# Optimization experiments

Hardware: AMD Instinct MI355X
Metric: run time of the kernel (lower is better)

The kernel has to match this reference:

```python
import jax, jax.numpy as jnp
import numpy as np

DN = ('NCHW', 'OIHW', 'NCHW')
B, T, D, H, W = 8, 10, 10, 128, 128
WINDOW_OUT = 5


def conv2d(x, w, b):
    y = jax.lax.conv_general_dilated(x, w, (1, 1), 'SAME', dimension_numbers=DN)
    return y + b[None, :, None, None]


def lstm_cell(x, h, c, w, b):
    # ConvLSTM gate update: conv over [x; h], split into i,f,o,g
    z = conv2d(jnp.concatenate([x, h], axis=1), w, b)
    i, f, o, g = jnp.split(z, 4, axis=1)
    c2 = jax.nn.sigmoid(f) * c + jax.nn.sigmoid(i) * jnp.tanh(g)
    h2 = jax.nn.sigmoid(o) * jnp.tanh(c2)
    return h2, c2


def attn_score(x, h, c, w1, b1, w2, b2):
    # conv-MLP attention score over concat([x, h, c]) -> (b, H, W)
    z = jnp.concatenate([x, h, c], axis=1)
    return conv2d(jnp.tanh(conv2d(z, w1, b1)), w2, b2)[:, 0]


def setup_inputs():
    key = jax.random.key(0)
    ks = jax.random.split(key, 16)
    s = 0.05
    return {
        'x': jax.random.normal(ks[0], (B, T, D, H, W), jnp.float32),
        'h0': jnp.zeros((B, 1, H, W), jnp.float32),
        'c0': jnp.zeros((B, 1, H, W), jnp.float32),
        'h1': jnp.zeros((B, 64, H, W), jnp.float32),
        'c1': jnp.zeros((B, 64, H, W), jnp.float32),
        # encoder cells: layer0 (in 10, hid 1), layer1 (in 1, hid 64)
        'w_enc0': jax.random.normal(ks[1], (4, 11, 3, 3), jnp.float32) * s,
        'b_enc0': jax.random.normal(ks[2], (4,), jnp.float32) * s,
        'w_enc1': jax.random.normal(ks[3], (256, 65, 3, 3), jnp.float32) * s,
        'b_enc1': jax.random.normal(ks[4], (256,), jnp.float32) * s,
        # decoder cells: layer0 (in 1, hid 64), layer1 (in 64, hid 1)
        'w_dec0': jax.random.normal(ks[5], (256, 65, 3, 3), jnp.float32) * s,
        'b_dec0': jax.random.normal(ks[6], (256,), jnp.float32) * s,
        'w_dec1': jax.random.normal(ks[7], (4, 65, 3, 3), jnp.float32) * s,
        'b_dec1': jax.random.normal(ks[8], (4,), jnp.float32) * s,
        # input attention: in 10+2*1=12 -> 32 -> 1
        'wa1': jax.random.normal(ks[9], (32, 12, 3, 3), jnp.float32) * s,
        'ba1': jax.random.normal(ks[10], (32,), jnp.float32) * s,
        'wa2': jax.random.normal(ks[11], (1, 32, 3, 3), jnp.float32) * s,
        'ba2': jax.random.normal(ks[12], (1,), jnp.float32) * s,
        # temporal attention: in 1+2*64=129 -> 32 -> 1
        'wt1': jax.random.normal(ks[13], (32, 129, 3, 3), jnp.float32) * s,
        'bt1': jax.random.normal(ks[14], (32,), jnp.float32) * s,
        'wt2': jax.random.normal(ks[15], (1, 32, 3, 3), jnp.float32) * s,
        'bt2': jnp.zeros((1,), jnp.float32),
    }


def reference(x, h0, c0, h1, c1, w_enc0, b_enc0, w_enc1, b_enc1,
              w_dec0, b_dec0, w_dec1, b_dec1,
              wa1, ba1, wa2, ba2, wt1, bt1, wt2, bt2):
    def input_attn(xx, h, c):
        # per-feature score; vmap over feature dim k (axis 2 of x)
        score = jax.vmap(lambda xk: attn_score(xk, h, c, wa1, ba1, wa2, ba2),
                         in_axes=2, out_axes=1)(xx)          # (b, D, H, W)
        alpha = jax.nn.softmax(score, axis=1)
        return xx * alpha[:, None]                            # broadcast over time

    # ---- encoder layer 0: input attention re-weights x every step (compounding)
    def step0(carry, t):
        xx, h, c = carry
        xx = input_attn(xx, h, c)
        h, c = lstm_cell(xx[:, t], h, c, w_enc0, b_enc0)
        return (xx, h, c), (h, c)

    _, (hs0, cs0) = jax.lax.scan(step0, (x, h0, c0), jnp.arange(T))
    hs0 = jnp.moveaxis(hs0, 0, 1)   # (b, T, 1, H, W)
    cs0 = jnp.moveaxis(cs0, 0, 1)

    # ---- encoder layer 1
    def step1(carry, xt):
        h, c = lstm_cell(xt, carry[0], carry[1], w_enc1, b_enc1)
        return (h, c), (h, c)

    _, (hs1, cs1) = jax.lax.scan(step1, (h1, c1), jnp.moveaxis(hs0, 1, 0))
    hs1 = jnp.moveaxis(hs1, 0, 1)   # (b, T, 64, H, W)
    cs1 = jnp.moveaxis(cs1, 0, 1)

    def temporal_attn(y, hb, cb):
        score = jax.vmap(lambda ht, ct: attn_score(y, ht, ct, wt1, bt1, wt2, bt2),
                         in_axes=1, out_axes=1)(hb, cb)       # (b, T, H, W)
        beta = jax.nn.softmax(score, axis=1)
        return jnp.sum(hb * beta[:, :, None], axis=1), cb[:, -1]

    # ---- decoder: states reversed -> layer0 uses encoder layer1 states, etc.
    y0 = x[:, -1, 0][:, None]       # x[:, [-1], selected_dim] -> (b, 1, H, W)

    def dec_step(carry, _):
        y, hb0, cb0, hb1, cb1 = carry
        ht, ct = temporal_attn(y, hb0, cb0)
        ht, ct = lstm_cell(y, ht, ct, w_dec0, b_dec0)
        y = ht
        hb0 = jnp.concatenate([hb0[:, 1:], ht[:, None]], axis=1)
        cb0 = jnp.concatenate([cb0[:, 1:], ct[:, None]], axis=1)
        ht2, ct2 = lstm_cell(y, hb1[:, -1], cb1[:, -1], w_dec1, b_dec1)
        y = ht2
        hb1 = jnp.concatenate([hb1[:, 1:], ht2[:, None]], axis=1)
        cb1 = jnp.concatenate([cb1[:, 1:], ct2[:, None]], axis=1)
        return (y, hb0, cb0, hb1, cb1), y

    _, ys = jax.lax.scan(dec_step, (y0, hs1, cs1, hs0, cs0), None, length=WINDOW_OUT)
    return jnp.moveaxis(ys, 0, 1)   # (b, window_out, 1, H, W)
```

## Files before the change

kernel.cpp:

```cpp
#include <hip/hip_runtime.h>


#define PX 16384L
#define T_ 10
#define D_ 10

__device__ __forceinline__ float fast_tanh(float x) {
    const float e = __builtin_exp2f(x * 2.88539008f);
    return 1.f - 2.f * __builtin_amdgcn_rcpf(e + 1.f);
}
__device__ __forceinline__ float fast_sig(float x) {
    const float e = __builtin_exp2f(x * -1.44269504f);
    return __builtin_amdgcn_rcpf(e + 1.f);
}
__device__ __forceinline__ float fast_exp(float x) {
    return __builtin_exp2f(x * 1.44269504f);
}

__device__ __forceinline__ void lstm_dev(
    float* lds,
    int tile, int hcb, int b,
    const float* __restrict__ in0, long bs0,
    const float* __restrict__ in1,
    const float* __restrict__ w, const float* __restrict__ bias,
    const float* __restrict__ cprev,
    float* __restrict__ hout, float* __restrict__ cout_)
{
    const int tid = threadIdx.x;
    const int tx = tid & 31, r0 = (tid >> 5) << 1;
    const int tileX = (tile & 3) << 5, tileY = (tile >> 2) << 4;
    const int hc0 = hcb << 1;
    float acc[16];
#pragma unroll
    for (int j = 0; j < 16; j++) acc[j] = 0.f;

    int g0[3]; float m0[3];
#pragma unroll
    for (int i = 0; i < 3; i++) {
        const int lidx = tid + i * 256;
        const int r = lidx / 34, cc = lidx - r * 34;
        const int gy = tileY + r - 1, gx = tileX + cc - 1;
        const bool inb = (lidx < 612) && ((unsigned)gy < 128u) && ((unsigned)gx < 128u);
        g0[i] = inb ? gy * 128 + gx : 0;
        m0[i] = inb ? 1.f : 0.f;
    }

    for (int cb = 0; cb < 65; cb += 8) {
        const int cmax = min(8, 65 - cb);
        for (int cl = 0; cl < cmax; cl++) {
            const int ci = cb + cl;
            const float* p = (ci == 0) ? in0 + (long)b * bs0
                                       : in1 + ((long)b * 64 + (ci - 1)) * PX;
#pragma unroll
            for (int i = 0; i < 3; i++) {
                const int lidx = tid + i * 256;
                if (lidx < 612) lds[cl * 612 + lidx] = m0[i] * p[g0[i]];
            }
        }
        __syncthreads();
        for (int cl = 0; cl < cmax; cl++) {
            float win[4][3];
#pragma unroll
            for (int dy = 0; dy < 4; dy++)
#pragma unroll
                for (int dx = 0; dx < 3; dx++)
                    win[dy][dx] = lds[cl * 612 + (r0 + dy) * 34 + tx + dx];
            const int ci = cb + cl;
#pragma unroll
            for (int j = 0; j < 2; j++)
#pragma unroll
                for (int g = 0; g < 4; g++) {
                    const float* wp = w + ((long)(g * 64 + hc0 + j) * 65 + ci) * 9;
#pragma unroll
                    for (int rr = 0; rr < 2; rr++) {
                        float a = acc[(j * 4 + g) * 2 + rr];
#pragma unroll
                        for (int ky = 0; ky < 3; ky++)
#pragma unroll
                            for (int kx = 0; kx < 3; kx++)
                                a = fmaf(wp[ky * 3 + kx], win[rr + ky][kx], a);
                        acc[(j * 4 + g) * 2 + rr] = a;
                    }
                }
        }
        __syncthreads();
    }
#pragma unroll
    for (int j = 0; j < 2; j++) {
        const int hc = hc0 + j;
        const float bi = bias[hc], bf = bias[64 + hc];
        const float bo = bias[128 + hc], bg = bias[192 + hc];
#pragma unroll
        for (int rr = 0; rr < 2; rr++) {
            const long opix = (long)(tileY + r0 + rr) * 128 + tileX + tx;
            const float i_ = fast_sig(acc[(j * 4 + 0) * 2 + rr] + bi);
            const float f_ = fast_sig(acc[(j * 4 + 1) * 2 + rr] + bf);
            const float o_ = fast_sig(acc[(j * 4 + 2) * 2 + rr] + bo);
            const float g_ = fast_tanh(acc[(j * 4 + 3) * 2 + rr] + bg);
            const float cp = cprev[((long)b * 64 + hc) * PX + opix];
            const float c2 = f_ * cp + i_ * g_;
            const float h2 = o_ * fast_tanh(c2);
            hout[((long)b * 64 + hc) * PX + opix] = h2;
            cout_[((long)b * 64 + hc) * PX + opix] = c2;
        }
    }
}

__device__ __forceinline__ void zpart_dev(
    float* lds,
    int tile, int cob, int b,
    const float* __restrict__ hsrc, const float* __restrict__ csrc,
    const float* __restrict__ wt1, const float* __restrict__ bt1,
    float* __restrict__ zdst)
{
    const int tid = threadIdx.x;
    const int tx = tid & 15, ty = tid >> 4;
    const int tileX = (tile & 7) << 4, tileY = (tile >> 3) << 4;
    const int co0 = cob << 3;
    float acc[8];
#pragma unroll
    for (int j = 0; j < 8; j++) acc[j] = 0.f;

    int g0[2]; float m0[2];
#pragma unroll
    for (int i = 0; i < 2; i++) {
        const int lidx = tid + i * 256;
        const int r = lidx / 18, cc = lidx - r * 18;
        const int gy = tileY + r - 1, gx = tileX + cc - 1;
        const bool inb = (lidx < 324) && ((unsigned)gy < 128u) && ((unsigned)gx < 128u);
        g0[i] = inb ? gy * 128 + gx : 0;
        m0[i] = inb ? 1.f : 0.f;
    }

    for (int cb = 0; cb < 128; cb += 4) {
        for (int cl = 0; cl < 4; cl++) {
            const int ci = cb + cl;
            const float* p = (ci < 64) ? hsrc + ((long)b * 64 + ci) * PX
                                       : csrc + ((long)b * 64 + (ci - 64)) * PX;
#pragma unroll
            for (int i = 0; i < 2; i++) {
                const int lidx = tid + i * 256;
                if (lidx < 324) lds[cl * 324 + lidx] = m0[i] * p[g0[i]];
            }
        }
        __syncthreads();
        for (int cl = 0; cl < 4; cl++) {
            float r9[9];
#pragma unroll
            for (int dy = 0; dy < 3; dy++)
#pragma unroll
                for (int dx = 0; dx < 3; dx++)
                    r9[dy * 3 + dx] = lds[cl * 324 + (ty + dy) * 18 + tx + dx];
            const int ci = cb + cl;
#pragma unroll
            for (int j = 0; j < 8; j++) {
                const float* wp = wt1 + ((long)(co0 + j) * 129 + 1 + ci) * 9;
                float a = acc[j];
#pragma unroll
                for (int q = 0; q < 9; q++) a = fmaf(wp[q], r9[q], a);
                acc[j] = a;
            }
        }
        __syncthreads();
    }
    const long opix = (long)(tileY + ty) * 128 + tileX + tx;
#pragma unroll
    for (int j = 0; j < 8; j++)
        zdst[((long)b * 32 + co0 + j) * PX + opix] = acc[j] + bt1[co0 + j];
}

__global__ __launch_bounds__(256)
void lstm_merge_k(const float* __restrict__ in0, long bs0,
                  const float* __restrict__ in1,
                  const float* __restrict__ w, const float* __restrict__ bias,
                  const float* __restrict__ cprev,
                  float* __restrict__ hout, float* __restrict__ cout_,
                  const float* __restrict__ zh, const float* __restrict__ zc,
                  float* __restrict__ zdst,
                  const float* __restrict__ wt1, const float* __restrict__ bt1)
{
    __shared__ float lds[8 * 612];
    const int bid = blockIdx.x, b = blockIdx.z;
    if (bid < 1024) {
        lstm_dev(lds, bid & 31, bid >> 5, b, in0, bs0, in1, w, bias,
                 cprev, hout, cout_);
    } else {
        const int q = bid - 1024;
        zpart_dev(lds, q & 63, q >> 6, b, zh, zc, wt1, bt1, zdst);
    }
}

__global__ __launch_bounds__(256)
void zpart_k(const float* __restrict__ zh, const float* __restrict__ zc,
             float* __restrict__ zdst,
             const float* __restrict__ wt1, const float* __restrict__ bt1)
{
    __shared__ float lds[4 * 324];
    zpart_dev(lds, blockIdx.x, blockIdx.y, blockIdx.z, zh, zc, wt1, bt1, zdst);
}

__global__ __launch_bounds__(256)
void dec_merge_k(const float* __restrict__ hs1s,
                 const float* __restrict__ hb1, long hb1bs,
                 const float* __restrict__ w1,
                 float* __restrict__ l1p, int nb,
                 const float* __restrict__ zc, float* __restrict__ zdst,
                 const float* __restrict__ wt1, const float* __restrict__ bt1)
{
    __shared__ float lds[4 * 324];
    const int bid = blockIdx.x, b = blockIdx.z;
    if (bid < 256) {
        const int tile = bid & 63, s = bid >> 6;
        const int ci0 = (s == 0) ? 0 : (s == 1) ? 17 : (s == 2) ? 33 : 49;
        const int cn  = (s == 0) ? 17 : 16;
        const int tid = threadIdx.x;
        const int tx = tid & 15, ty = tid >> 4;
        const int tileX = (tile & 7) << 4, tileY = (tile >> 3) << 4;
        int g0[2]; float m0[2];
#pragma unroll
        for (int i = 0; i < 2; i++) {
            const int lidx = tid + i * 256;
            const int r = lidx / 18, cc = lidx - r * 18;
            const int gy = tileY + r - 1, gx = tileX + cc - 1;
            const bool inb = (lidx < 324) && ((unsigned)gy < 128u) && ((unsigned)gx < 128u);
            g0[i] = inb ? gy * 128 + gx : 0;
            m0[i] = inb ? 1.f : 0.f;
        }
        float acc[4] = {0.f, 0.f, 0.f, 0.f};
        for (int cb = 0; cb < cn; cb += 4) {
            const int cmax = min(4, cn - cb);
            for (int cl = 0; cl < cmax; cl++) {
                const int ci = ci0 + cb + cl;
                const float* p = (ci < 64) ? hs1s + ((long)b * 64 + ci) * PX
                                           : hb1 + (long)b * hb1bs;
#pragma unroll
                for (int i = 0; i < 2; i++) {
                    const int lidx = tid + i * 256;
                    if (lidx < 324) lds[cl * 324 + lidx] = m0[i] * p[g0[i]];
                }
            }
            __syncthreads();
            for (int cl = 0; cl < cmax; cl++) {
                float r9[9];
#pragma unroll
                for (int dy = 0; dy < 3; dy++)
#pragma unroll
                    for (int dx = 0; dx < 3; dx++)
                        r9[dy * 3 + dx] = lds[cl * 324 + (ty + dy) * 18 + tx + dx];
                const int ci = ci0 + cb + cl;
#pragma unroll
                for (int j = 0; j < 4; j++) {
                    const float* wp = w1 + ((long)j * 65 + ci) * 9;
                    float a = acc[j];
#pragma unroll
                    for (int q = 0; q < 9; q++) a = fmaf(wp[q], r9[q], a);
                    acc[j] = a;
                }
            }
            __syncthreads();
        }
        const long opix = (long)(tileY + ty) * 128 + tileX + tx;
#pragma unroll
        for (int j = 0; j < 4; j++)
            l1p[(((long)s * nb + b) * 4 + j) * PX + opix] = acc[j];
    } else {
        const int q = bid - 256;
        zpart_dev(lds, q & 63, q >> 6, b, hs1s, zc, wt1, bt1, zdst);
    }
}

__global__ __launch_bounds__(256)
void combine_lstm_k(const float* __restrict__ pbuf, int nsl, int hidden,
                    const float* __restrict__ bias,
                    const float* __restrict__ cprev, long cpbs,
                    float* __restrict__ hout, long hobs,
                    float* __restrict__ cout_, long cobs,
                    float* __restrict__ hout2, long ho2bs, int nb)
{
    const long idx = (long)blockIdx.x * 256 + threadIdx.x;
    if (idx >= (long)nb * hidden * PX) return;
    const long px = idx & 16383;
    const long v = idx >> 14;
    const int hc = (int)(v % hidden), b = (int)(v / hidden);
    const int nco = 4 * hidden;
    float g4[4] = {0.f, 0.f, 0.f, 0.f};
    for (int s = 0; s < nsl; s++)
#pragma unroll
        for (int g = 0; g < 4; g++)
            g4[g] += pbuf[(((long)s * nb + b) * nco + g * hidden + hc) * PX + px];
    const float i_ = fast_sig(g4[0] + bias[hc]);
    const float f_ = fast_sig(g4[1] + bias[hidden + hc]);
    const float o_ = fast_sig(g4[2] + bias[2 * hidden + hc]);
    const float g_ = fast_tanh(g4[3] + bias[3 * hidden + hc]);
    const float cp = cprev[(long)b * cpbs + (long)hc * PX + px];
    const float c2 = f_ * cp + i_ * g_;
    const float h2 = o_ * fast_tanh(c2);
    hout[(long)b * hobs + (long)hc * PX + px] = h2;
    cout_[(long)b * cobs + (long)hc * PX + px] = c2;
    if (hout2) hout2[(long)b * ho2bs + (long)hc * PX + px] = h2;
}

__global__ __launch_bounds__(256)
void enc0_lstm_k(const float* __restrict__ x, int t, const float* __restrict__ A,
                 const float* __restrict__ hprev, const float* __restrict__ cprev,
                 const float* __restrict__ w, const float* __restrict__ bias,
                 float* __restrict__ hout, float* __restrict__ cout_)
{
    __shared__ float lds[4 * 324];
    const int tid = threadIdx.x;
    const int tx = tid & 15, ty = tid >> 4;
    const int tile = blockIdx.x, b = blockIdx.z;
    const int tileX = (tile & 7) << 4, tileY = (tile >> 3) << 4;
    int g0[2]; float m0[2]; float aTr[2][10];
#pragma unroll
    for (int i = 0; i < 2; i++) {
        const int lidx = tid + i * 256;
        const int r = lidx / 18, cc = lidx - r * 18;
        const int gy = tileY + r - 1, gx = tileX + cc - 1;
        const bool inb = (lidx < 324) && ((unsigned)gy < 128u) && ((unsigned)gx < 128u);
        g0[i] = inb ? gy * 128 + gx : 0;
        m0[i] = inb ? 1.f : 0.f;
    }
    float acc[4] = {0.f, 0.f, 0.f, 0.f};
    for (int cb = 0; cb < 11; cb += 4) {
        const int cmax = min(4, 11 - cb);
        for (int cl = 0; cl < cmax; cl++) {
            const int ci = cb + cl;
#pragma unroll
            for (int i = 0; i < 2; i++) {
                const int lidx = tid + i * 256;
                if (lidx < 324) {
                    float v;
                    if (ci < 10) {
                        v = x[(((long)b * T_ + t) * D_ + ci) * PX + g0[i]]
                            * A[((long)b * 10 + ci) * PX + g0[i]];
                    } else {
                        v = hprev[(long)b * PX + g0[i]];
                    }
                    lds[cl * 324 + lidx] = m0[i] * v;
                }
            }
        }
        __syncthreads();
        for (int cl = 0; cl < cmax; cl++) {
            float r9[9];
#pragma unroll
            for (int dy = 0; dy < 3; dy++)
#pragma unroll
                for (int dx = 0; dx < 3; dx++)
                    r9[dy * 3 + dx] = lds[cl * 324 + (ty + dy) * 18 + tx + dx];
            const int ci = cb + cl;
#pragma unroll
            for (int g = 0; g < 4; g++) {
                const float* wp = w + ((long)g * 11 + ci) * 9;
                float a = acc[g];
#pragma unroll
                for (int q = 0; q < 9; q++) a = fmaf(wp[q], r9[q], a);
                acc[g] = a;
            }
        }
        __syncthreads();
    }
    const long opix = (long)(tileY + ty) * 128 + tileX + tx;
    const float i_ = fast_sig(acc[0] + bias[0]);
    const float f_ = fast_sig(acc[1] + bias[1]);
    const float o_ = fast_sig(acc[2] + bias[2]);
    const float g_ = fast_tanh(acc[3] + bias[3]);
    const float cp = cprev[(long)b * PX + opix];
    const float c2 = f_ * cp + i_ * g_;
    const float h2 = o_ * fast_tanh(c2);
    hout[(long)b * PX + opix] = h2;
    cout_[(long)b * PX + opix] = c2;
}

__global__ __launch_bounds__(256)
void iattn_k(const float* __restrict__ x, const float* __restrict__ A,
             const float* __restrict__ h, const float* __restrict__ c,
             const float* __restrict__ wa1, const float* __restrict__ ba1,
             const float* __restrict__ wa2, const float* __restrict__ ba2,
             float* __restrict__ score)
{
    __shared__ float xl[12][400];
    __shared__ float zl[16][324];
    const int tid = threadIdx.x;
    const int tileX = (blockIdx.x & 7) << 4, tileY = (blockIdx.x >> 3) << 4;
    const int z = blockIdx.z;
    const int b = z & 7, k = z >> 3;

    int g0[2]; float m0[2]; float aTr[2];
#pragma unroll
    for (int i = 0; i < 2; i++) {
        const int lidx = tid + i * 256;
        const int r = lidx / 20, cc = lidx - r * 20;
        const int gy = tileY + r - 2, gx = tileX + cc - 2;
        const bool inb = (lidx < 400) && ((unsigned)gy < 128u) && ((unsigned)gx < 128u);
        g0[i] = inb ? gy * 128 + gx : 0;
        m0[i] = inb ? 1.f : 0.f;
        aTr[i] = A ? (m0[i] * A[((long)b * 10 + k) * PX + g0[i]]) : 1.f;
    }
    for (int ch = 0; ch < 12; ch++) {
        const float* p = (ch < 10) ? x + (((long)b * 10 + ch) * 10 + k) * PX
                       : (ch == 10) ? h + (long)b * PX : c + (long)b * PX;
#pragma unroll
        for (int i = 0; i < 2; i++) {
            const int lidx = tid + i * 256;
            if (lidx < 400) {
                float v = m0[i] * p[g0[i]];
                if (ch < 10) v *= aTr[i];
                xl[ch][lidx] = v;
            }
        }
    }
    __syncthreads();

    const int i0 = tid;
    const int i1 = tid + 256;
    const int zr0 = i0 / 18, zc0 = i0 - zr0 * 18;
    const int zr1 = (i1 < 324) ? i1 / 18 : 0;
    const int zc1 = (i1 < 324) ? i1 - zr1 * 18 : 0;
    const int gy0 = tileY + zr0 - 1, gx0 = tileX + zc0 - 1;
    const bool in0_ = (i0 < 324) && ((unsigned)gy0 < 128u) && ((unsigned)gx0 < 128u);
    const int gy1 = tileY + zr1 - 1, gx1 = tileX + zc1 - 1;
    const bool in1_ = (i1 < 324) && ((unsigned)gy1 < 128u) && ((unsigned)gx1 < 128u);

    const int tx = tid & 15, ty = tid >> 4;
    float sacc = ba2[0];

    for (int hf = 0; hf < 2; hf++) {
        float acc0[16], acc1[16];
#pragma unroll
        for (int co = 0; co < 16; co++) { acc0[co] = 0.f; acc1[co] = 0.f; }
        for (int ci = 0; ci < 12; ci++) {
            float wA[9], wB[9];
#pragma unroll
            for (int dy = 0; dy < 3; dy++)
#pragma unroll
                for (int dx = 0; dx < 3; dx++) {
                    wA[dy * 3 + dx] = xl[ci][(zr0 + dy) * 20 + zc0 + dx];
                    wB[dy * 3 + dx] = xl[ci][(zr1 + dy) * 20 + zc1 + dx];
                }
#pragma unroll
            for (int co = 0; co < 16; co++) {
                const float* wp = wa1 + ((long)(hf * 16 + co) * 12 + ci) * 9;
                float a0 = acc0[co], a1 = acc1[co];
#pragma unroll
                for (int q = 0; q < 9; q++) {
                    a0 = fmaf(wp[q], wA[q], a0);
                    a1 = fmaf(wp[q], wB[q], a1);
                }
                acc0[co] = a0; acc1[co] = a1;
            }
        }
        if (hf) __syncthreads();
#pragma unroll
        for (int co = 0; co < 16; co++) {
            zl[co][i0] = in0_ ? fast_tanh(acc0[co] + ba1[hf * 16 + co]) : 0.f;
            if (i1 < 324) zl[co][i1] = in1_ ? fast_tanh(acc1[co] + ba1[hf * 16 + co]) : 0.f;
        }
        __syncthreads();
        for (int co = 0; co < 16; co++) {
            const float* wp = wa2 + (hf * 16 + co) * 9;
#pragma unroll
            for (int ky = 0; ky < 3; ky++)
#pragma unroll
                for (int kx = 0; kx < 3; kx++)
                    sacc = fmaf(wp[ky * 3 + kx], zl[co][(ty + ky) * 18 + tx + kx], sacc);
        }
    }
    score[((long)b * 10 + k) * PX + (long)(tileY + ty) * 128 + tileX + tx] = sacc;
}

__global__ __launch_bounds__(256)
void softmax_mul_k(const float* __restrict__ s, float* __restrict__ A, int nb, int init)
{
    const long idx = (long)blockIdx.x * 256 + threadIdx.x;
    if (idx >= (long)nb * PX) return;
    const long b = idx >> 14, p = idx & 16383;
    const float* base = s + b * 10 * PX + p;
    float v[10]; float m = -1e30f;
#pragma unroll
    for (int t = 0; t < 10; t++) { v[t] = base[t * PX]; m = fmaxf(m, v[t]); }
    float sum = 0.f;
#pragma unroll
    for (int t = 0; t < 10; t++) { v[t] = fast_exp(v[t] - m); sum += v[t]; }
    const float r = __builtin_amdgcn_rcpf(sum);
    float* Ab = A + b * 10 * PX + p;
#pragma unroll
    for (int t = 0; t < 10; t++)
        Ab[t * PX] = init ? (v[t] * r) : (Ab[t * PX] * v[t] * r);
}

__global__ __launch_bounds__(256)
void attn_fuse_k(const float* __restrict__ y, long ybs,
                 const float* __restrict__ zpart,
                 const float* __restrict__ wt1,
                 const float* __restrict__ wt2, const float* __restrict__ bt2,
                 float* __restrict__ score, int nb)
{
    __shared__ float ylds[400];
    __shared__ float zl[16][324];
    const int tid = threadIdx.x;
    const int tileX = (blockIdx.x & 7) << 4, tileY = (blockIdx.x >> 3) << 4;
    const int z = blockIdx.z;
    const int b = z % nb, t = z / nb;

#pragma unroll
    for (int i = 0; i < 2; i++) {
        const int lidx = tid + i * 256;
        if (lidx < 400) {
            const int r = lidx / 20, cc = lidx - r * 20;
            const int gy = tileY + r - 2, gx = tileX + cc - 2;
            const bool inb = ((unsigned)gy < 128u) && ((unsigned)gx < 128u);
            ylds[lidx] = inb ? y[(long)b * ybs + gy * 128 + gx] : 0.f;
        }
    }
    __syncthreads();

    const int i0 = tid, i1 = tid + 256;
    const int zr0 = i0 / 18, zc0 = i0 - zr0 * 18;
    const int zr1 = (i1 < 324) ? i1 / 18 : 0;
    const int zc1 = (i1 < 324) ? i1 - zr1 * 18 : 0;
    const int gy0 = tileY + zr0 - 1, gx0 = tileX + zc0 - 1;
    const bool in0_ = ((unsigned)gy0 < 128u) && ((unsigned)gx0 < 128u);
    const int gy1 = tileY + zr1 - 1, gx1 = tileX + zc1 - 1;
    const bool in1_ = (i1 < 324) && ((unsigned)gy1 < 128u) && ((unsigned)gx1 < 128u);
    const long pix0 = in0_ ? (long)gy0 * 128 + gx0 : 0;
    const long pix1 = in1_ ? (long)gy1 * 128 + gx1 : 0;
    const float* zp0 = zpart + ((long)t * nb + b) * 32 * PX;

    const int tx = tid & 15, ty = tid >> 4;
    float sacc = bt2[0];

    for (int hf = 0; hf < 2; hf++) {
        float yw0[9], yw1[9];
#pragma unroll
        for (int dy = 0; dy < 3; dy++)
#pragma unroll
            for (int dx = 0; dx < 3; dx++) {
                yw0[dy * 3 + dx] = ylds[(zr0 + dy) * 20 + zc0 + dx];
                yw1[dy * 3 + dx] = ylds[(zr1 + dy) * 20 + zc1 + dx];
            }
        if (hf) __syncthreads();
#pragma unroll 4
        for (int ch = 0; ch < 16; ch++) {
            const int cg = hf * 16 + ch;
            const float* wy = wt1 + (long)cg * 129 * 9;
            float s0 = zp0[(long)cg * PX + pix0];
            float s1 = (i1 < 324) ? zp0[(long)cg * PX + pix1] : 0.f;
#pragma unroll
            for (int q = 0; q < 9; q++) {
                s0 = fmaf(wy[q], yw0[q], s0);
                s1 = fmaf(wy[q], yw1[q], s1);
            }
            zl[ch][i0] = in0_ ? fast_tanh(s0) : 0.f;
            if (i1 < 324) zl[ch][i1] = in1_ ? fast_tanh(s1) : 0.f;
        }
        __syncthreads();
        for (int ch = 0; ch < 16; ch++) {
            const float* wp = wt2 + (hf * 16 + ch) * 9;
#pragma unroll
            for (int ky = 0; ky < 3; ky++)
#pragma unroll
                for (int kx = 0; kx < 3; kx++)
                    sacc = fmaf(wp[ky * 3 + kx], zl[ch][(ty + ky) * 18 + tx + kx], sacc);
        }
    }
    score[((long)b * 10 + t) * PX + (long)(tileY + ty) * 128 + tileX + tx] = sacc;
}

__global__ __launch_bounds__(256)
void smax_wsum_k(const float* __restrict__ score, const float* __restrict__ hs1,
                 float* __restrict__ aht, int nb)
{
    const long idx = (long)blockIdx.x * 256 + threadIdx.x;
    if (idx >= (long)nb * PX) return;
    const long b = idx >> 14, p = idx & 16383;
    const int ch0 = blockIdx.y * 8;
    const float* base = score + b * 10 * PX + p;
    float v[10]; float m = -1e30f;
#pragma unroll
    for (int t = 0; t < 10; t++) { v[t] = base[t * PX]; m = fmaxf(m, v[t]); }
    float sum = 0.f;
#pragma unroll
    for (int t = 0; t < 10; t++) { v[t] = fast_exp(v[t] - m); sum += v[t]; }
    const float r = __builtin_amdgcn_rcpf(sum);
#pragma unroll
    for (int t = 0; t < 10; t++) v[t] *= r;
    const long slot1 = (long)nb * 64 * PX;
#pragma unroll
    for (int j = 0; j < 8; j++) {
        const int ch = ch0 + j;
        float a = 0.f;
#pragma unroll
        for (int t = 0; t < 10; t++)
            a += v[t] * hs1[t * slot1 + (b * 64 + ch) * PX + p];
        aht[(b * 64 + ch) * PX + p] = a;
    }
}

extern "C" void kernel_launch(void* const* d_in, const int* in_sizes, int n_in,
                              void* d_out, int out_size, void* d_ws, size_t ws_size,
                              hipStream_t stream)
{
    const float* x      = (const float*)d_in[0];
    const float* h0     = (const float*)d_in[1];
    const float* c0in   = (const float*)d_in[2];
    const float* h1     = (const float*)d_in[3];
    const float* c1     = (const float*)d_in[4];
    const float* w_enc0 = (const float*)d_in[5];
    const float* b_enc0 = (const float*)d_in[6];
    const float* w_enc1 = (const float*)d_in[7];
    const float* b_enc1 = (const float*)d_in[8];
    const float* w_dec0 = (const float*)d_in[9];
    const float* b_dec0 = (const float*)d_in[10];
    const float* w_dec1 = (const float*)d_in[11];
    const float* b_dec1 = (const float*)d_in[12];
    const float* wa1 = (const float*)d_in[13];
    const float* ba1 = (const float*)d_in[14];
    const float* wa2 = (const float*)d_in[15];
    const float* ba2 = (const float*)d_in[16];
    const float* wt1 = (const float*)d_in[17];
    const float* bt1 = (const float*)d_in[18];
    const float* wt2 = (const float*)d_in[19];
    const float* bt2 = (const float*)d_in[20];
    float* out = (float*)d_out;

    int nb = 0;
    for (int cand = 8; cand >= 1; cand >>= 1) {
        const size_t need = (size_t)(160 + 1188 * cand) * PX * sizeof(float);
        if (need <= ws_size) { nb = cand; break; }
    }
    if (nb == 0) return;

    float* ws = (float*)d_ws;
    float* hs0 = ws;
    float* cs0 = hs0 + 80 * PX;
    float* G   = cs0 + 80 * PX;
    float* A    = G;
    float* sc1  = G + 80 * PX;
    const long slot1  = (long)nb * 64 * PX;
    float* hs1   = G;
    float* cs1   = hs1 + 10 * slot1;
    float* zpart = cs1 + 2 * slot1;
    float* aht   = zpart + (long)10 * nb * 32 * PX;
    float* l1p   = aht + (long)nb * 64 * PX;
    float* hs0g  = l1p + (long)4 * nb * 4 * PX;
    float* cs0g  = hs0g + (long)5 * nb * PX;
    float* scD   = cs0g + (long)5 * nb * PX;

    const dim3 blk(256);
    const long TDP = (long)T_ * D_ * PX;
    const long zslot = (long)nb * 32 * PX;

    for (int t = 0; t < 10; t++) {
        const float* hprev = (t == 0) ? h0 : hs0 + (long)(t - 1) * 8 * PX;
        const float* cprev = (t == 0) ? c0in : cs0 + (long)(t - 1) * 8 * PX;
        iattn_k<<<dim3(64, 1, 80), blk, 0, stream>>>(
            x, (t == 0) ? nullptr : A, hprev, cprev, wa1, ba1, wa2, ba2, sc1);
        softmax_mul_k<<<512, blk, 0, stream>>>(sc1, A, 8, t == 0);
        enc0_lstm_k<<<dim3(64, 1, 8), blk, 0, stream>>>(
            x, t, A, hprev, cprev, w_enc0, b_enc0,
            hs0 + (long)t * 8 * PX, cs0 + (long)t * 8 * PX);
    }

    for (int b0 = 0; b0 < 8; b0 += nb) {
        const float* xb  = x + (long)b0 * TDP;
        float* outb = out + (long)b0 * 5 * PX;

        for (int t = 0; t < 10; t++) {
            const float* hprev = (t == 0) ? h1 + (long)b0 * 64 * PX
                                          : hs1 + (long)(t - 1) * slot1;
            const float* cprev = (t == 0) ? c1 + (long)b0 * 64 * PX
                                          : cs1 + (long)((t - 1) & 1) * slot1;
            const int gx = (t == 0) ? 1024 : 1280;
            lstm_merge_k<<<dim3(gx, 1, nb), blk, 0, stream>>>(
                hs0 + (long)t * 8 * PX + (long)b0 * PX, PX,
                hprev, w_enc1, b_enc1, cprev,
                hs1 + (long)t * slot1, cs1 + (long)(t & 1) * slot1,
                (t == 0) ? nullptr : hs1 + (long)(t - 1) * slot1,
                (t == 0) ? nullptr : cs1 + (long)((t - 1) & 1) * slot1,
                (t == 0) ? nullptr : zpart + (long)(t - 1) * zslot,
                wt1, bt1);
        }
        zpart_k<<<dim3(64, 4, nb), blk, 0, stream>>>(
            hs1 + 9L * slot1, cs1 + slot1, zpart + 9L * zslot, wt1, bt1);

        for (int s = 0; s < 5; s++) {
            const float* yptr; long ybs;
            if (s == 0) { yptr = xb + 9L * D_ * PX; ybs = TDP; }
            else        { yptr = hs0g + (long)(s - 1) * nb * PX; ybs = PX; }
            const float* hb1 = (s == 0) ? hs0 + 9L * 8 * PX + (long)b0 * PX
                                        : hs0g + (long)(s - 1) * nb * PX;
            const float* cb1 = (s == 0) ? cs0 + 9L * 8 * PX + (long)b0 * PX
                                        : cs0g + (long)(s - 1) * nb * PX;

            attn_fuse_k<<<dim3(64, 1, 10 * nb), blk, 0, stream>>>(
                yptr, ybs, zpart, wt1, wt2, bt2, scD, nb);
            smax_wsum_k<<<dim3((int)(((long)nb * PX + 255) / 256), 8), blk, 0, stream>>>(
                scD, hs1, aht, nb);

            lstm_merge_k<<<dim3(1024, 1, nb), blk, 0, stream>>>(
                yptr, ybs, aht, w_dec0, b_dec0,
                cs1 + (long)((s + 1) & 1) * slot1,
                hs1 + (long)s * slot1, cs1 + (long)(s & 1) * slot1,
                nullptr, nullptr, nullptr, wt1, bt1);

            const int gx2 = (s < 4) ? 512 : 256;
            dec_merge_k<<<dim3(gx2, 1, nb), blk, 0, stream>>>(
                hs1 + (long)s * slot1, hb1, PX, w_dec1, l1p, nb,
                cs1 + (long)(s & 1) * slot1, zpart + (long)s * zslot, wt1, bt1);
            combine_lstm_k<<<(int)(((long)nb * PX + 255) / 256), blk, 0, stream>>>(
                l1p, 4, 1, b_dec1, cb1, PX,
                hs0g + (long)s * nb * PX, PX,
                cs0g + (long)s * nb * PX, PX,
                outb + (long)s * PX, 5 * PX, nb);
        }
    }
}
```

Before: 21.86 ms.

## Widen conv register blocking, fuse input softmax into enc0, split tail work

Each lstm_dev block now computes 4 hidden channels and each zpart block 16 output channels, doubling per-thread register accumulation to reuse LDS windows and cut block count. The separate softmax_mul kernel is removed: enc0_lstm recomputes the softmax inline for its halo pixels and extra blocks write the updated attention into a ping-pong buffer. The attention kernels split the second-pixel work so that only the 68 threads that have one compute it, instead of predicating inside a shared loop. Higher register pressure may lower occupancy, and the dec_merge grid size changed while the kernel body appears untouched.

Result: slower. 24.50 ms (+12.1%).

```diff
diff --git a/kernel.cpp b/kernel.cpp
--- a/kernel.cpp
+++ b/kernel.cpp
@@ -29,10 +29,10 @@
     const int tid = threadIdx.x;
     const int tx = tid & 31, r0 = (tid >> 5) << 1;
     const int tileX = (tile & 3) << 5, tileY = (tile >> 2) << 4;
-    const int hc0 = hcb << 1;
-    float acc[16];
-#pragma unroll
-    for (int j = 0; j < 16; j++) acc[j] = 0.f;
+    const int hc0 = hcb << 2;
+    float acc[32];
+#pragma unroll
+    for (int j = 0; j < 32; j++) acc[j] = 0.f;
 
     int g0[3]; float m0[3];
 #pragma unroll
@@ -67,7 +67,7 @@
                     win[dy][dx] = lds[cl * 612 + (r0 + dy) * 34 + tx + dx];
             const int ci = cb + cl;
 #pragma unroll
-            for (int j = 0; j < 2; j++)
+            for (int j = 0; j < 4; j++)
 #pragma unroll
                 for (int g = 0; g < 4; g++) {
                     const float* wp = w + ((long)(g * 64 + hc0 + j) * 65 + ci) * 9;
@@ -86,7 +86,7 @@
         __syncthreads();
     }
 #pragma unroll
-    for (int j = 0; j < 2; j++) {
+    for (int j = 0; j < 4; j++) {
         const int hc = hc0 + j;
         const float bi = bias[hc], bf = bias[64 + hc];
         const float bo = bias[128 + hc], bg = bias[192 + hc];
@@ -116,10 +116,10 @@
     const int tid = threadIdx.x;
     const int tx = tid & 15, ty = tid >> 4;
     const int tileX = (tile & 7) << 4, tileY = (tile >> 3) << 4;
-    const int co0 = cob << 3;
-    float acc[8];
-#pragma unroll
-    for (int j = 0; j < 8; j++) acc[j] = 0.f;
+    const int co0 = cob << 4;
+    float acc[16];
+#pragma unroll
+    for (int j = 0; j < 16; j++) acc[j] = 0.f;
 
     int g0[2]; float m0[2];
 #pragma unroll
@@ -153,7 +153,7 @@
                     r9[dy * 3 + dx] = lds[cl * 324 + (ty + dy) * 18 + tx + dx];
             const int ci = cb + cl;
 #pragma unroll
-            for (int j = 0; j < 8; j++) {
+            for (int j = 0; j < 16; j++) {
                 const float* wp = wt1 + ((long)(co0 + j) * 129 + 1 + ci) * 9;
                 float a = acc[j];
 #pragma unroll
@@ -165,7 +165,7 @@
     }
     const long opix = (long)(tileY + ty) * 128 + tileX + tx;
 #pragma unroll
-    for (int j = 0; j < 8; j++)
+    for (int j = 0; j < 16; j++)
         zdst[((long)b * 32 + co0 + j) * PX + opix] = acc[j] + bt1[co0 + j];
 }
 
@@ -181,11 +181,11 @@
 {
     __shared__ float lds[8 * 612];
     const int bid = blockIdx.x, b = blockIdx.z;
-    if (bid < 1024) {
+    if (bid < 512) {
         lstm_dev(lds, bid & 31, bid >> 5, b, in0, bs0, in1, w, bias,
                  cprev, hout, cout_);
     } else {
-        const int q = bid - 1024;
+        const int q = bid - 512;
         zpart_dev(lds, q & 63, q >> 6, b, zh, zc, wt1, bt1, zdst);
     }
 }
@@ -301,17 +301,38 @@
 }
 
 __global__ __launch_bounds__(256)
-void enc0_lstm_k(const float* __restrict__ x, int t, const float* __restrict__ A,
+void enc0_lstm_k(const float* __restrict__ x, int t,
+                 const float* __restrict__ Acur, float* __restrict__ Anext,
+                 const float* __restrict__ sc1,
                  const float* __restrict__ hprev, const float* __restrict__ cprev,
                  const float* __restrict__ w, const float* __restrict__ bias,
                  float* __restrict__ hout, float* __restrict__ cout_)
 {
     __shared__ float lds[4 * 324];
     const int tid = threadIdx.x;
+    const int b = blockIdx.z;
+    if (blockIdx.x >= 64) {
+        const long p = (((long)blockIdx.x - 64) << 8) + tid;
+        const float* sp = sc1 + (long)b * 10 * PX + p;
+        float v[10]; float m = -1e30f;
+#pragma unroll
+        for (int k = 0; k < 10; k++) { v[k] = sp[k * PX]; m = fmaxf(m, v[k]); }
+        float sum = 0.f;
+#pragma unroll
+        for (int k = 0; k < 10; k++) { v[k] = fast_exp(v[k] - m); sum += v[k]; }
+        const float r = __builtin_amdgcn_rcpf(sum);
+        float* Ap = Anext + (long)b * 10 * PX + p;
+#pragma unroll
+        for (int k = 0; k < 10; k++) {
+            const float a = v[k] * r;
+            Ap[k * PX] = Acur ? Acur[((long)b * 10 + k) * PX + p] * a : a;
+        }
+        return;
+    }
     const int tx = tid & 15, ty = tid >> 4;
-    const int tile = blockIdx.x, b = blockIdx.z;
+    const int tile = blockIdx.x;
     const int tileX = (tile & 7) << 4, tileY = (tile >> 3) << 4;
-    int g0[2]; float m0[2]; float aTr[2][10];
+    int g0[2]; float m0[2]; float e[2][10]; float rr_[2];
 #pragma unroll
     for (int i = 0; i < 2; i++) {
         const int lidx = tid + i * 256;
@@ -320,43 +341,58 @@
         const bool inb = (lidx < 324) && ((unsigned)gy < 128u) && ((unsigned)gx < 128u);
         g0[i] = inb ? gy * 128 + gx : 0;
         m0[i] = inb ? 1.f : 0.f;
+        const float* sp = sc1 + (long)b * 10 * PX + g0[i];
+        float mm = -1e30f;
+#pragma unroll
+        for (int k = 0; k < 10; k++) { e[i][k] = sp[k * PX]; mm = fmaxf(mm, e[i][k]); }
+        float sum = 0.f;
+#pragma unroll
+        for (int k = 0; k < 10; k++) { e[i][k] = fast_exp(e[i][k] - mm); sum += e[i][k]; }
+        rr_[i] = __builtin_amdgcn_rcpf(sum);
     }
     float acc[4] = {0.f, 0.f, 0.f, 0.f};
+#pragma unroll
     for (int cb = 0; cb < 11; cb += 4) {
-        const int cmax = min(4, 11 - cb);
-        for (int cl = 0; cl < cmax; cl++) {
+#pragma unroll
+        for (int cl = 0; cl < 4; cl++) {
             const int ci = cb + cl;
-#pragma unroll
-            for (int i = 0; i < 2; i++) {
-                const int lidx = tid + i * 256;
-                if (lidx < 324) {
-                    float v;
-                    if (ci < 10) {
-                        v = x[(((long)b * T_ + t) * D_ + ci) * PX + g0[i]]
-                            * A[((long)b * 10 + ci) * PX + g0[i]];
-                    } else {
-                        v = hprev[(long)b * PX + g0[i]];
+            if (ci < 11) {
+#pragma unroll
+                for (int i = 0; i < 2; i++) {
+                    const int lidx = tid + i * 256;
+                    if (lidx < 324) {
+                        float vv;
+                        if (ci < 10) {
+                            float al = e[i][ci] * rr_[i];
+                            if (Acur) al *= Acur[((long)b * 10 + ci) * PX + g0[i]];
+                            vv = x[(((long)b * T_ + t) * D_ + ci) * PX + g0[i]] * al;
+                        } else {
+                            vv = hprev[(long)b * PX + g0[i]];
+                        }
+                        lds[cl * 324 + lidx] = m0[i] * vv;
                     }
-                    lds[cl * 324 + lidx] = m0[i] * v;
                 }
             }
         }
         __syncthreads();
-        for (int cl = 0; cl < cmax; cl++) {
-            float r9[9];
-#pragma unroll
-            for (int dy = 0; dy < 3; dy++)
-#pragma unroll
-                for (int dx = 0; dx < 3; dx++)
-                    r9[dy * 3 + dx] = lds[cl * 324 + (ty + dy) * 18 + tx + dx];
+#pragma unroll
+        for (int cl = 0; cl < 4; cl++) {
             const int ci = cb + cl;
-#pragma unroll
-            for (int g = 0; g < 4; g++) {
-                const float* wp = w + ((long)g * 11 + ci) * 9;
-                float a = acc[g];
-#pragma unroll
-                for (int q = 0; q < 9; q++) a = fmaf(wp[q], r9[q], a);
-                acc[g] = a;
+            if (ci < 11) {
+                float r9[9];
+#pragma unroll
+                for (int dy = 0; dy < 3; dy++)
+#pragma unroll
+                    for (int dx = 0; dx < 3; dx++)
+                        r9[dy * 3 + dx] = lds[cl * 324 + (ty + dy) * 18 + tx + dx];
+#pragma unroll
+                for (int g = 0; g < 4; g++) {
+                    const float* wp = w + ((long)g * 11 + ci) * 9;
+                    float a = acc[g];
+#pragma unroll
+                    for (int q = 0; q < 9; q++) a = fmaf(wp[q], r9[q], a);
+                    acc[g] = a;
+                }
             }
         }
         __syncthreads();
@@ -419,7 +455,7 @@
     const int zr1 = (i1 < 324) ? i1 / 18 : 0;
     const int zc1 = (i1 < 324) ? i1 - zr1 * 18 : 0;
     const int gy0 = tileY + zr0 - 1, gx0 = tileX + zc0 - 1;
-    const bool in0_ = (i0 < 324) && ((unsigned)gy0 < 128u) && ((unsigned)gx0 < 128u);
+    const bool in0_ = ((unsigned)gy0 < 128u) && ((unsigned)gx0 < 128u);
     const int gy1 = tileY + zr1 - 1, gx1 = tileX + zc1 - 1;
     const bool in1_ = (i1 < 324) && ((unsigned)gy1 < 128u) && ((unsigned)gx1 < 128u);
 
@@ -427,35 +463,54 @@
     float sacc = ba2[0];
 
     for (int hf = 0; hf < 2; hf++) {
-        float acc0[16], acc1[16];
-#pragma unroll
-        for (int co = 0; co < 16; co++) { acc0[co] = 0.f; acc1[co] = 0.f; }
+        float acc0[16];
+#pragma unroll
+        for (int co = 0; co < 16; co++) acc0[co] = 0.f;
         for (int ci = 0; ci < 12; ci++) {
-            float wA[9], wB[9];
+            float wA[9];
 #pragma unroll
             for (int dy = 0; dy < 3; dy++)
 #pragma unroll
-                for (int dx = 0; dx < 3; dx++) {
+                for (int dx = 0; dx < 3; dx++)
                     wA[dy * 3 + dx] = xl[ci][(zr0 + dy) * 20 + zc0 + dx];
-                    wB[dy * 3 + dx] = xl[ci][(zr1 + dy) * 20 + zc1 + dx];
-                }
 #pragma unroll
             for (int co = 0; co < 16; co++) {
                 const float* wp = wa1 + ((long)(hf * 16 + co) * 12 + ci) * 9;
-                float a0 = acc0[co], a1 = acc1[co];
-#pragma unroll
-                for (int q = 0; q < 9; q++) {
-                    a0 = fmaf(wp[q], wA[q], a0);
-                    a1 = fmaf(wp[q], wB[q], a1);
+                float a0 = acc0[co];
+#pragma unroll
+                for (int q = 0; q < 9; q++) a0 = fmaf(wp[q], wA[q], a0);
+                acc0[co] = a0;
+            }
+        }
+        float acc1[16];
+        if (tid < 68) {
+#pragma unroll
+            for (int co = 0; co < 16; co++) acc1[co] = 0.f;
+            for (int ci = 0; ci < 12; ci++) {
+                float wB[9];
+#pragma unroll
+                for (int dy = 0; dy < 3; dy++)
+#pragma unroll
+                    for (int dx = 0; dx < 3; dx++)
+                        wB[dy * 3 + dx] = xl[ci][(zr1 + dy) * 20 + zc1 + dx];
+#pragma unroll
+                for (int co = 0; co < 16; co++) {
+                    const float* wp = wa1 + ((long)(hf * 16 + co) * 12 + ci) * 9;
+                    float a1 = acc1[co];
+#pragma unroll
+                    for (int q = 0; q < 9; q++) a1 = fmaf(wp[q], wB[q], a1);
+                    acc1[co] = a1;
                 }
-                acc0[co] = a0; acc1[co] = a1;
             }
         }
         if (hf) __syncthreads();
 #pragma unroll
-        for (int co = 0; co < 16; co++) {
+        for (int co = 0; co < 16; co++)
             zl[co][i0] = in0_ ? fast_tanh(acc0[co] + ba1[hf * 16 + co]) : 0.f;
-            if (i1 < 324) zl[co][i1] = in1_ ? fast_tanh(acc1[co] + ba1[hf * 16 + co]) : 0.f;
+        if (tid < 68) {
+#pragma unroll
+            for (int co = 0; co < 16; co++)
+                zl[co][i1] = in1_ ? fast_tanh(acc1[co] + ba1[hf * 16 + co]) : 0.f;
         }
         __syncthreads();
         for (int co = 0; co < 16; co++) {
@@ -468,26 +523,6 @@
         }
     }
     score[((long)b * 10 + k) * PX + (long)(tileY + ty) * 128 + tileX + tx] = sacc;
-}
-
-__global__ __launch_bounds__(256)
-void softmax_mul_k(const float* __restrict__ s, float* __restrict__ A, int nb, int init)
-{
-    const long idx = (long)blockIdx.x * 256 + threadIdx.x;
-    if (idx >= (long)nb * PX) return;
-    const long b = idx >> 14, p = idx & 16383;
-    const float* base = s + b * 10 * PX + p;
-    float v[10]; float m = -1e30f;
-#pragma unroll
-    for (int t = 0; t < 10; t++) { v[t] = base[t * PX]; m = fmaxf(m, v[t]); }
-    float sum = 0.f;
-#pragma unroll
-    for (int t = 0; t < 10; t++) { v[t] = fast_exp(v[t] - m); sum += v[t]; }
-    const float r = __builtin_amdgcn_rcpf(sum);
-    float* Ab = A + b * 10 * PX + p;
-#pragma unroll
-    for (int t = 0; t < 10; t++)
-        Ab[t * PX] = init ? (v[t] * r) : (Ab[t * PX] * v[t] * r);
 }
 
 __global__ __launch_bounds__(256)
@@ -532,28 +567,38 @@
     float sacc = bt2[0];
 
     for (int hf = 0; hf < 2; hf++) {
-        float yw0[9], yw1[9];
+        float yw0[9];
 #pragma unroll
         for (int dy = 0; dy < 3; dy++)
 #pragma unroll
-            for (int dx = 0; dx < 3; dx++) {
+            for (int dx = 0; dx < 3; dx++)
                 yw0[dy * 3 + dx] = ylds[(zr0 + dy) * 20 + zc0 + dx];
-                yw1[dy * 3 + dx] = ylds[(zr1 + dy) * 20 + zc1 + dx];
-            }
         if (hf) __syncthreads();
 #pragma unroll 4
         for (int ch = 0; ch < 16; ch++) {
             const int cg = hf * 16 + ch;
             const float* wy = wt1 + (long)cg * 129 * 9;
             float s0 = zp0[(long)cg * PX + pix0];
-            float s1 = (i1 < 324) ? zp0[(long)cg * PX + pix1] : 0.f;
-#pragma unroll
-            for (int q = 0; q < 9; q++) {
-                s0 = fmaf(wy[q], yw0[q], s0);
-                s1 = fmaf(wy[q], yw1[q], s1);
-            }
+#pragma unroll
+            for (int q = 0; q < 9; q++) s0 = fmaf(wy[q], yw0[q], s0);
             zl[ch][i0] = in0_ ? fast_tanh(s0) : 0.f;
-            if (i1 < 324) zl[ch][i1] = in1_ ? fast_tanh(s1) : 0.f;
+        }
+        if (tid < 68) {
+            float yw1[9];
+#pragma unroll
+            for (int dy = 0; dy < 3; dy++)
+#pragma unroll
+                for (int dx = 0; dx < 3; dx++)
+                    yw1[dy * 3 + dx] = ylds[(zr1 + dy) * 20 + zc1 + dx];
+#pragma unroll 4
+            for (int ch = 0; ch < 16; ch++) {
+                const int cg = hf * 16 + ch;
+                const float* wy = wt1 + (long)cg * 129 * 9;
+                float s1 = zp0[(long)cg * PX + pix1];
+#pragma unroll
+                for (int q = 0; q < 9; q++) s1 = fmaf(wy[q], yw1[q], s1);
+                zl[ch][i1] = in1_ ? fast_tanh(s1) : 0.f;
+            }
         }
         __syncthreads();
         for (int ch = 0; ch < 16; ch++) {
@@ -636,8 +681,9 @@
     float* hs0 = ws;
     float* cs0 = hs0 + 80 * PX;
     float* G   = cs0 + 80 * PX;
-    float* A    = G;
-    float* sc1  = G + 80 * PX;
+    float* Abuf0 = G;
+    float* Abuf1 = G + 80 * PX;
+    float* sc1   = G + 160 * PX;
     const long slot1  = (long)nb * 64 * PX;
     float* hs1   = G;
     float* cs1   = hs1 + 10 * slot1;
@@ -655,11 +701,12 @@
     for (int t = 0; t < 10; t++) {
         const float* hprev = (t == 0) ? h0 : hs0 + (long)(t - 1) * 8 * PX;
         const float* cprev = (t == 0) ? c0in : cs0 + (long)(t - 1) * 8 * PX;
+        const float* Acur  = (t == 0) ? nullptr : ((t & 1) ? Abuf1 : Abuf0);
+        float* Anext = (t & 1) ? Abuf0 : Abuf1;
         iattn_k<<<dim3(64, 1, 80), blk, 0, stream>>>(
-            x, (t == 0) ? nullptr : A, hprev, cprev, wa1, ba1, wa2, ba2, sc1);
-        softmax_mul_k<<<512, blk, 0, stream>>>(sc1, A, 8, t == 0);
-        enc0_lstm_k<<<dim3(64, 1, 8), blk, 0, stream>>>(
-            x, t, A, hprev, cprev, w_enc0, b_enc0,
+            x, Acur, hprev, cprev, wa1, ba1, wa2, ba2, sc1);
+        enc0_lstm_k<<<dim3(128, 1, 8), blk, 0, stream>>>(
+            x, t, Acur, Anext, sc1, hprev, cprev, w_enc0, b_enc0,
             hs0 + (long)t * 8 * PX, cs0 + (long)t * 8 * PX);
     }
 
@@ -672,7 +719,7 @@
                                           : hs1 + (long)(t - 1) * slot1;
             const float* cprev = (t == 0) ? c1 + (long)b0 * 64 * PX
                                           : cs1 + (long)((t - 1) & 1) * slot1;
-            const int gx = (t == 0) ? 1024 : 1280;
+            const int gx = (t == 0) ? 512 : 640;
             lstm_merge_k<<<dim3(gx, 1, nb), blk, 0, stream>>>(
                 hs0 + (long)t * 8 * PX + (long)b0 * PX, PX,
                 hprev, w_enc1, b_enc1, cprev,
@@ -682,7 +729,7 @@
                 (t == 0) ? nullptr : zpart + (long)(t - 1) * zslot,
                 wt1, bt1);
         }
-        zpart_k<<<dim3(64, 4, nb), blk, 0, stream>>>(
+        zpart_k<<<dim3(64, 2, nb), blk, 0, stream>>>(
             hs1 + 9L * slot1, cs1 + slot1, zpart + 9L * zslot, wt1, bt1);
 
         for (int s = 0; s < 5; s++) {
@@ -699,13 +746,13 @@
             smax_wsum_k<<<dim3((int)(((long)nb * PX + 255) / 256), 8), blk, 0, stream>>>(
                 scD, hs1, aht, nb);
 
-            lstm_merge_k<<<dim3(1024, 1, nb), blk, 0, stream>>>(
+            lstm_merge_k<<<dim3(512, 1, nb), blk, 0, stream>>>(
                 yptr, ybs, aht, w_dec0, b_dec0,
                 cs1 + (long)((s + 1) & 1) * slot1,
                 hs1 + (long)s * slot1, cs1 + (long)(s & 1) * slot1,
                 nullptr, nullptr, nullptr, wt1, bt1);
 
-            const int gx2 = (s < 4) ? 512 : 256;
+            const int gx2 = (s < 4) ? 384 : 256;
             dec_merge_k<<<dim3(gx2, 1, nb), blk, 0, stream>>>(
                 hs1 + (long)s * slot1, hb1, PX, w_dec1, l1p, nb,
                 cs1 + (long)(s & 1) * slot1, zpart + (long)s * zslot, wt1, bt1);
```
